# Performance work log

Hardware: AMD Instinct MI355X
Metric: run time of the kernel (lower is better)

The kernel has to match this reference:

```python
import jax, jax.numpy as jnp
import numpy as np

TILE = 16


def _tiled_hamilton_transform(tiles, weights):
    """tiles: [B, T, 16, 4]; weights: [T, 16, 16, 4] -> [B, T, 16, 4].

    Equivalent to broadcasting the Hamilton product to [B,T,16,16,4] and
    summing over dim=2, but expressed as 16 small einsum contractions so the
    large intermediate is never materialized.
    """
    a1, b1, c1, d1 = [tiles[..., k] for k in range(4)]      # each [B, T, 16]
    a2, b2, c2, d2 = [weights[..., k] for k in range(4)]    # each [T, 16, 16]

    def ctr(x, w):
        return jnp.einsum('bti,tij->btj', x, w)

    r_a = ctr(a1, a2) - ctr(b1, b2) - ctr(c1, c2) - ctr(d1, d2)
    r_b = ctr(a1, b2) + ctr(b1, a2) + ctr(c1, d2) - ctr(d1, c2)
    r_c = ctr(a1, c2) - ctr(b1, d2) + ctr(c1, a2) + ctr(d1, b2)
    r_d = ctr(a1, d2) + ctr(b1, c2) - ctr(c1, b2) + ctr(d1, a2)
    return jnp.stack([r_a, r_b, r_c, r_d], axis=-1)


def setup_inputs() -> dict:
    key = jax.random.key(0)
    k1, k2, k3 = jax.random.split(key, 3)
    x = jax.random.normal(k1, (65536, 256, 4), dtype=jnp.float32)
    phi_weights = jax.random.normal(k2, (16, 16, 16, 4), dtype=jnp.float32) * 0.02
    psi_weights = jax.random.normal(k3, (16, 16, 16, 4), dtype=jnp.float32) * 0.02
    return {"x": x, "phi_weights": phi_weights, "psi_weights": psi_weights}


def reference(x, phi_weights, psi_weights):
    B, D, _ = x.shape                      # D = manifold_dim = 256
    half_tiles = D // 2 // TILE            # = 8 = num_tiles // 2
    x1, x2 = jnp.split(x, 2, axis=1)       # each [B, 128, 4]
    x1_tiles = x1.reshape(B, half_tiles, TILE, 4)
    x2_tiles = x2.reshape(B, half_tiles, TILE, 4)

    f_out = _tiled_hamilton_transform(x2_tiles, phi_weights[:half_tiles])
    y1_tiles = x1_tiles + f_out
    g_out = _tiled_hamilton_transform(y1_tiles, psi_weights[half_tiles:])
    y2_tiles = x2_tiles + g_out

    y1 = y1_tiles.reshape(B, -1, 4)
    y2 = y2_tiles.reshape(B, -1, 4)
    return jnp.concatenate([y1, y2], axis=1)
```

## Files before the change

### kernel.cpp

```cpp
#include <hip/hip_runtime.h>
#include <hip/hip_bf16.h>


typedef __attribute__((ext_vector_type(8))) short bf16x8;
typedef __attribute__((ext_vector_type(4))) float f32x4;

static __device__ __forceinline__ unsigned short f2bf(float f) {
    unsigned u = __builtin_bit_cast(unsigned, f);
    unsigned r = 0x7FFFu + ((u >> 16) & 1u);
    return (unsigned short)((u + r) >> 16);
}

static __device__ __forceinline__ short hwbf(float f) {
    __hip_bfloat16 h = __float2bfloat16(f);
    return __builtin_bit_cast(short, h);
}

__global__ __launch_bounds__(256)
void prep_kernel(const float4* __restrict__ phi,
                 const float4* __restrict__ psi,
                 unsigned short* __restrict__ mt) {
    __shared__ float Phi[64][64];
    __shared__ float Psi[64][64];
    const int t   = blockIdx.x;
    const int tid = threadIdx.x;
    const int i   = tid >> 4, j = tid & 15;

    {
        float4 w = phi[t * 256 + i * 16 + j];
        float a = w.x, b = w.y, c = w.z, d = w.w;
        Phi[4*i+0][4*j+0]= a; Phi[4*i+0][4*j+1]= b; Phi[4*i+0][4*j+2]= c; Phi[4*i+0][4*j+3]= d;
        Phi[4*i+1][4*j+0]=-b; Phi[4*i+1][4*j+1]= a; Phi[4*i+1][4*j+2]=-d; Phi[4*i+1][4*j+3]= c;
        Phi[4*i+2][4*j+0]=-c; Phi[4*i+2][4*j+1]= d; Phi[4*i+2][4*j+2]= a; Phi[4*i+2][4*j+3]=-b;
        Phi[4*i+3][4*j+0]=-d; Phi[4*i+3][4*j+1]=-c; Phi[4*i+3][4*j+2]= b; Phi[4*i+3][4*j+3]= a;
        float4 v = psi[(8 + t) * 256 + i * 16 + j];
        a = v.x; b = v.y; c = v.z; d = v.w;
        Psi[4*i+0][4*j+0]= a; Psi[4*i+0][4*j+1]= b; Psi[4*i+0][4*j+2]= c; Psi[4*i+0][4*j+3]= d;
        Psi[4*i+1][4*j+0]=-b; Psi[4*i+1][4*j+1]= a; Psi[4*i+1][4*j+2]=-d; Psi[4*i+1][4*j+3]= c;
        Psi[4*i+2][4*j+0]=-c; Psi[4*i+2][4*j+1]= d; Psi[4*i+2][4*j+2]= a; Psi[4*i+2][4*j+3]=-b;
        Psi[4*i+3][4*j+0]=-d; Psi[4*i+3][4*j+1]=-c; Psi[4*i+3][4*j+2]= b; Psi[4*i+3][4*j+3]= a;
    }
    __syncthreads();

    unsigned short* m = mt + t * 16384;
    for (int e = tid; e < 16384; e += 256) {
        const int n = e >> 7, k = e & 127;
        if (n >= 64 && k >= 64) continue;
        float v;
        if (k < 64 && n < 64)       v = (k == n) ? 1.f : 0.f;
        else if (k >= 64)           v = Phi[k - 64][n];
        else                        v = Psi[k][n - 64];
        m[e] = f2bf(v);
    }
    const int r = tid & 63, c0 = (tid >> 6) * 16;
    float pk[16];
#pragma unroll
    for (int cc = 0; cc < 16; ++cc) pk[cc] = 0.f;
    for (int k = 0; k < 64; ++k) {
        const float fr = Phi[r][k];
#pragma unroll
        for (int cc = 0; cc < 16; ++cc) pk[cc] = fmaf(fr, Psi[k][c0 + cc], pk[cc]);
    }
#pragma unroll
    for (int cc = 0; cc < 16; ++cc) {
        const int c = c0 + cc;
        m[(64 + c) * 128 + (64 + r)] = f2bf(((r == c) ? 1.f : 0.f) + pk[cc]);
    }
}

__global__ __launch_bounds__(512, 4)
void gemm_kernel(const float* __restrict__ x,
                 const unsigned short* __restrict__ mt,
                 float* __restrict__ out,
                 int nchunks) {
    __shared__ __align__(16) char inbuf[2][16384];
    __shared__ __align__(16) char outbuf[32768];

    const int tid  = threadIdx.x;
    const int tg   = blockIdx.x & 1;
    const int bc   = blockIdx.x >> 1;
    const int cs   = gridDim.x >> 1;
    const int lane = tid & 63, w = tid >> 6;
    const int twl  = w >> 1, hw = w & 1;
    const int twg  = tg * 4 + twl;
    const int ln = lane & 15, lk = lane >> 4;

    bf16x8 a[4][4];
    {
        const unsigned short* mtt = mt + twg * 16384;
#pragma unroll
        for (int fn = 0; fn < 4; ++fn)
#pragma unroll
            for (int ks = 0; ks < 4; ++ks)
                a[fn][ks] = *(const bf16x8*)(mtt + (hw*64 + fn*16 + ln)*128
                                                 + ks*32 + lk*8);
    }

    const int sr    = tid >> 5;
    const int sp    = tid & 31;
    const int shalf = sp >> 4;
    const int sseg  = sp & 15;
    const size_t gcb = (size_t)(shalf ? 512 : 0) + tg * 256 + sseg * 4;
    const int swz   = (sr & 7) << 4;

    float4 L[4];
#define ISSUE(cc) { \
        const float* xr = x + ((size_t)(cc) * 16 + sr) * 1024 + gcb; \
        L[0] = *(const float4*)(xr);        L[1] = *(const float4*)(xr + 64); \
        L[2] = *(const float4*)(xr + 128);  L[3] = *(const float4*)(xr + 192); }

    int c = bc;
    if (c < nchunks) ISSUE(c)

    int cur = 0;
    while (c < nchunks) {
#pragma unroll
        for (int l = 0; l < 4; ++l) {
            short4 h;
            h.x = hwbf(L[l].x); h.y = hwbf(L[l].y);
            h.z = hwbf(L[l].z); h.w = hwbf(L[l].w);
            const int byte = (sr * 1024 + (shalf * 256 + sseg * 4 + l * 64) * 2) ^ swz;
            *(short4*)(inbuf[cur] + byte) = h;
        }
        __syncthreads();

        const int cn = c + cs;
        if (cn < nchunks) ISSUE(cn)

        f32x4 acc[4];
#pragma unroll
        for (int fn = 0; fn < 4; ++fn) acc[fn] = (f32x4)(0.f);
#pragma unroll
        for (int ks = 0; ks < 4; ++ks) {
            const int lcol = (ks < 2) ? (twl * 64 + ks * 32 + lk * 8)
                                      : (256 + twl * 64 + (ks - 2) * 32 + lk * 8);
            const int byte = (ln * 1024 + lcol * 2) ^ ((ln & 7) << 4);
            const bf16x8 bx = *(const bf16x8*)(inbuf[cur] + byte);
#pragma unroll
            for (int fn = 0; fn < 4; ++fn)
                acc[fn] = __builtin_amdgcn_mfma_f32_16x16x32_bf16(
                    a[fn][ks], bx, acc[fn], 0, 0, 0);
        }

#pragma unroll
        for (int fn = 0; fn < 4; ++fn) {
            const int lcolf = hw * 256 + twl * 64 + fn * 16 + lk * 4;
            const int byte  = (ln * 2048 + lcolf * 4) ^ ((ln & 7) << 4);
            *(f32x4*)(outbuf + byte) = acc[fn];
        }
        __syncthreads();

        {
            float* orow = out + ((size_t)c * 16 + sr) * 1024 + gcb;
#pragma unroll
            for (int l = 0; l < 4; ++l) {
                const int byte = (sr * 2048 + (shalf * 256 + sseg * 4 + l * 64) * 4) ^ swz;
                *(f32x4*)(orow + l * 64) = *(const f32x4*)(outbuf + byte);
            }
        }

        cur ^= 1;
        c = cn;
    }
#undef ISSUE
}

extern "C" void kernel_launch(void* const* d_in, const int* in_sizes, int n_in,
                              void* d_out, int out_size, void* d_ws, size_t ws_size,
                              hipStream_t stream) {
    const float* x    = (const float*)d_in[0];
    const float4* phi = (const float4*)d_in[1];
    const float4* psi = (const float4*)d_in[2];
    unsigned short* mt = (unsigned short*)d_ws;
    float* out = (float*)d_out;

    const int rows    = in_sizes[0] / 1024;
    const int nchunks = rows / 16;
    const int blocks  = 512;

    prep_kernel<<<8, 256, 0, stream>>>(phi, psi, mt);
    gemm_kernel<<<blocks, 512, 0, stream>>>(x, mt, out, nchunks);
}
```

Before: 118.0 us.

## Split gemm into four tile-pair blocks and store MFMA results directly

Each block now handles two tile pairs (256 threads, quarter of the columns) instead of four, launching 1024 blocks with half the shared input buffer. The output staging through shared memory and its second barrier are removed; accumulators are written straight to global memory. Input staging uses wider 16-byte bf16 stores. The direct stores are 16-byte segments scattered across rows, which may coalesce less well than the staged full-row writes.

```diff
diff --git a/kernel.cpp b/kernel.cpp
--- a/kernel.cpp
+++ b/kernel.cpp
@@ -68,21 +68,20 @@
     }
 }
 
-__global__ __launch_bounds__(512, 4)
+__global__ __launch_bounds__(256, 4)
 void gemm_kernel(const float* __restrict__ x,
                  const unsigned short* __restrict__ mt,
                  float* __restrict__ out,
                  int nchunks) {
-    __shared__ __align__(16) char inbuf[2][16384];
-    __shared__ __align__(16) char outbuf[32768];
+    __shared__ __align__(16) char inbuf[2][8192];
 
     const int tid  = threadIdx.x;
-    const int tg   = blockIdx.x & 1;
-    const int bc   = blockIdx.x >> 1;
-    const int cs   = gridDim.x >> 1;
+    const int pr   = blockIdx.x & 3;
+    const int bc   = blockIdx.x >> 2;
+    const int cs   = gridDim.x >> 2;
     const int lane = tid & 63, w = tid >> 6;
-    const int twl  = w >> 1, hw = w & 1;
-    const int twg  = tg * 4 + twl;
+    const int tw = w >> 1, hw = w & 1;
+    const int twg = pr * 2 + tw;
     const int ln = lane & 15, lk = lane >> 4;
 
     bf16x8 a[4][4];
@@ -96,31 +95,33 @@
                                                  + ks*32 + lk*8);
     }
 
-    const int sr    = tid >> 5;
-    const int sp    = tid & 31;
-    const int shalf = sp >> 4;
-    const int sseg  = sp & 15;
-    const size_t gcb = (size_t)(shalf ? 512 : 0) + tg * 256 + sseg * 4;
-    const int swz   = (sr & 7) << 4;
+    const int sr  = tid >> 4, seg = tid & 15;
+    const size_t gb  = (size_t)pr * 128 + seg * 8;
+    const int    swz = (sr & 7) << 4;
 
     float4 L[4];
 #define ISSUE(cc) { \
-        const float* xr = x + ((size_t)(cc) * 16 + sr) * 1024 + gcb; \
-        L[0] = *(const float4*)(xr);        L[1] = *(const float4*)(xr + 64); \
-        L[2] = *(const float4*)(xr + 128);  L[3] = *(const float4*)(xr + 192); }
+        const float* xr = x + ((size_t)(cc) * 16 + sr) * 1024 + gb; \
+        L[0] = *(const float4*)(xr);       L[1] = *(const float4*)(xr + 4); \
+        L[2] = *(const float4*)(xr + 512); L[3] = *(const float4*)(xr + 516); }
 
     int c = bc;
     if (c < nchunks) ISSUE(c)
 
     int cur = 0;
     while (c < nchunks) {
-#pragma unroll
-        for (int l = 0; l < 4; ++l) {
-            short4 h;
-            h.x = hwbf(L[l].x); h.y = hwbf(L[l].y);
-            h.z = hwbf(L[l].z); h.w = hwbf(L[l].w);
-            const int byte = (sr * 1024 + (shalf * 256 + sseg * 4 + l * 64) * 2) ^ swz;
-            *(short4*)(inbuf[cur] + byte) = h;
+        {
+            bf16x8 h0, h1;
+            h0[0] = hwbf(L[0].x); h0[1] = hwbf(L[0].y);
+            h0[2] = hwbf(L[0].z); h0[3] = hwbf(L[0].w);
+            h0[4] = hwbf(L[1].x); h0[5] = hwbf(L[1].y);
+            h0[6] = hwbf(L[1].z); h0[7] = hwbf(L[1].w);
+            h1[0] = hwbf(L[2].x); h1[1] = hwbf(L[2].y);
+            h1[2] = hwbf(L[2].z); h1[3] = hwbf(L[2].w);
+            h1[4] = hwbf(L[3].x); h1[5] = hwbf(L[3].y);
+            h1[6] = hwbf(L[3].z); h1[7] = hwbf(L[3].w);
+            *(bf16x8*)(inbuf[cur] + ((sr * 512 + seg * 16) ^ swz))       = h0;
+            *(bf16x8*)(inbuf[cur] + ((sr * 512 + 256 + seg * 16) ^ swz)) = h1;
         }
         __syncthreads();
 
@@ -132,30 +133,23 @@
         for (int fn = 0; fn < 4; ++fn) acc[fn] = (f32x4)(0.f);
 #pragma unroll
         for (int ks = 0; ks < 4; ++ks) {
-            const int lcol = (ks < 2) ? (twl * 64 + ks * 32 + lk * 8)
-                                      : (256 + twl * 64 + (ks - 2) * 32 + lk * 8);
-            const int byte = (ln * 1024 + lcol * 2) ^ ((ln & 7) << 4);
-            const bf16x8 bx = *(const bf16x8*)(inbuf[cur] + byte);
+            const int col = ((ks < 2) ? tw * 64 + ks * 32
+                                      : 128 + tw * 64 + (ks - 2) * 32) + lk * 8;
+            const bf16x8 bx = *(const bf16x8*)(inbuf[cur]
+                                + ((ln * 512 + col * 2) ^ ((ln & 7) << 4)));
 #pragma unroll
             for (int fn = 0; fn < 4; ++fn)
                 acc[fn] = __builtin_amdgcn_mfma_f32_16x16x32_bf16(
                     a[fn][ks], bx, acc[fn], 0, 0, 0);
         }
 
+        {
+            float* orow = out + ((size_t)c * 16 + ln) * 1024;
 #pragma unroll
-        for (int fn = 0; fn < 4; ++fn) {
-            const int lcolf = hw * 256 + twl * 64 + fn * 16 + lk * 4;
-            const int byte  = (ln * 2048 + lcolf * 4) ^ ((ln & 7) << 4);
-            *(f32x4*)(outbuf + byte) = acc[fn];
-        }
-        __syncthreads();
-
-        {
-            float* orow = out + ((size_t)c * 16 + sr) * 1024 + gcb;
-#pragma unroll
-            for (int l = 0; l < 4; ++l) {
-                const int byte = (sr * 2048 + (shalf * 256 + sseg * 4 + l * 64) * 4) ^ swz;
-                *(f32x4*)(orow + l * 64) = *(const f32x4*)(outbuf + byte);
+            for (int fn = 0; fn < 4; ++fn) {
+                const int colo = ((hw == 0) ? twg * 64 + fn * 16
+                                            : 512 + twg * 64 + fn * 16) + lk * 4;
+                *(f32x4*)(orow + colo) = acc[fn];
             }
         }
 
@@ -176,8 +170,8 @@
 
     const int rows    = in_sizes[0] / 1024;
     const int nchunks = rows / 16;
-    const int blocks  = 512;
+    const int blocks  = 4 * 256;
 
     prep_kernel<<<8, 256, 0, stream>>>(phi, psi, mt);
-    gemm_kernel<<<blocks, 512, 0, stream>>>(x, mt, out, nchunks);
+    gemm_kernel<<<blocks, 256, 0, stream>>>(x, mt, out, nchunks);
 }
```

Result: no change. 117.1 us (-0.8%).
